# Performance work log

Measured on AMD Instinct MI355X. Metric: run time of the kernel, lower is better.

The kernel has to match this reference:

```python
import jax, jax.numpy as jnp
import numpy as np

BLOCK = 32  # GGUF Q8_0 block size
O, I = 4096, 4096
NB = I // BLOCK  # blocks per output row
B, S = 2, 2048


def setup_inputs() -> dict:
    key = jax.random.key(0)
    k1, k2, k3, k4 = jax.random.split(key, 4)
    x = jax.random.normal(k1, (B, S, I), dtype=jnp.float32)
    # signed int8 quants stored as int32 (values in [-128, 127])
    q_weight = jax.random.randint(k2, (O, I), 0, 256, dtype=jnp.int32) - 128
    # per-block fp scales (small positive, as produced by Q8_0 quantization)
    scales = jax.random.uniform(k3, (O, NB), dtype=jnp.float32) * 0.02 + 1e-4
    bias = jax.random.normal(k4, (O,), dtype=jnp.float32)
    return {"x": x, "q_weight": q_weight, "scales": scales, "bias": bias}


def dequantize(q_weight, scales, dtype):
    # q_weight: [O, I] int, scales: [O, NB] float; block-wise dequant (Q8_0)
    q = q_weight.reshape(O, NB, BLOCK).astype(dtype)
    w = q * scales.astype(dtype)[:, :, None]
    return w.reshape(O, I)  # [O, I]


def reference(x, q_weight, scales, bias):
    # cast_bias_weight: dequantize weight/bias to the input dtype, then linear
    dtype = x.dtype
    w = dequantize(q_weight, scales, dtype)          # [O, I]
    y = jnp.einsum('bsi,oi->bso', x, w) + bias.astype(dtype)
    return y
```

## Files before the change

kernel.cpp:

```cpp
#include <hip/hip_runtime.h>
#include <hip/hip_bf16.h>
#include <stdint.h>


#define M_DIM 4096
#define N_DIM 4096
#define K_DIM 4096
#define NB_SC 128

#define BM 256
#define BN 256
#define BKB 128
#define NT (K_DIM / BKB)
#define TILE_B (BM * BKB)

typedef __attribute__((ext_vector_type(4))) int i32x4;

__device__ __forceinline__ void gload_lds16(const void* gsrc, void* ldsdst) {
  __builtin_amdgcn_global_load_lds(
      (__attribute__((address_space(1))) void*)(uintptr_t)gsrc,
      (__attribute__((address_space(3))) void*)(uint32_t)(uintptr_t)ldsdst,
      16, 0, 0);
}

__device__ __forceinline__ int pack4(int a, int b, int c, int d) {
  return (a & 255) | ((b & 255) << 8) | ((c & 255) << 16) | ((d & 255) << 24);
}


__global__ void prep_kernel(const float* __restrict__ x, const int* __restrict__ q,
                            const float* __restrict__ sc,
                            char* __restrict__ xb, char* __restrict__ wb,
                            float* __restrict__ sxv, float* __restrict__ swv) {
  __shared__ float red[4];
  const int b = blockIdx.x;
  const int t = threadIdx.x;
  if (b < 4096) {
    const float4* row = (const float4*)(x + (size_t)b * K_DIM);
    float4 v[4];
    float m = 0.f;
#pragma unroll
    for (int i = 0; i < 4; ++i) {
      v[i] = row[t * 4 + i];
      m = fmaxf(m, fmaxf(fmaxf(fabsf(v[i].x), fabsf(v[i].y)),
                         fmaxf(fabsf(v[i].z), fabsf(v[i].w))));
    }
#pragma unroll
    for (int off = 32; off >= 1; off >>= 1) m = fmaxf(m, __shfl_xor(m, off, 64));
    if ((t & 63) == 0) red[t >> 6] = m;
    __syncthreads();
    m = fmaxf(fmaxf(red[0], red[1]), fmaxf(red[2], red[3]));
    const float inv = (m > 0.f) ? 127.0f / m : 0.f;
    int4 o;
    o.x = pack4(__float2int_rn(v[0].x * inv), __float2int_rn(v[0].y * inv),
                __float2int_rn(v[0].z * inv), __float2int_rn(v[0].w * inv));
    o.y = pack4(__float2int_rn(v[1].x * inv), __float2int_rn(v[1].y * inv),
                __float2int_rn(v[1].z * inv), __float2int_rn(v[1].w * inv));
    o.z = pack4(__float2int_rn(v[2].x * inv), __float2int_rn(v[2].y * inv),
                __float2int_rn(v[2].z * inv), __float2int_rn(v[2].w * inv));
    o.w = pack4(__float2int_rn(v[3].x * inv), __float2int_rn(v[3].y * inv),
                __float2int_rn(v[3].z * inv), __float2int_rn(v[3].w * inv));
    ((int4*)(xb + (size_t)b * K_DIM))[t] = o;
    if (t == 0) sxv[b] = m / 127.0f;
  } else {
    const int o_row = b - 4096;
    float m = sc[o_row * NB_SC + (t & 127)];
#pragma unroll
    for (int off = 32; off >= 1; off >>= 1) m = fmaxf(m, __shfl_xor(m, off, 64));
    if ((t & 63) == 0) red[t >> 6] = m;
    __syncthreads();
    m = fmaxf(fmaxf(red[0], red[1]), fmaxf(red[2], red[3]));
    const float ratio = sc[o_row * NB_SC + (t >> 1)] / m;
    const int4* qp = (const int4*)(q + (size_t)o_row * K_DIM);
    int4 qv[4];
#pragma unroll
    for (int i = 0; i < 4; ++i) qv[i] = qp[t * 4 + i];
    int4 ov;
    ov.x = pack4(__float2int_rn((float)qv[0].x * ratio), __float2int_rn((float)qv[0].y * ratio),
                 __float2int_rn((float)qv[0].z * ratio), __float2int_rn((float)qv[0].w * ratio));
    ov.y = pack4(__float2int_rn((float)qv[1].x * ratio), __float2int_rn((float)qv[1].y * ratio),
                 __float2int_rn((float)qv[1].z * ratio), __float2int_rn((float)qv[1].w * ratio));
    ov.z = pack4(__float2int_rn((float)qv[2].x * ratio), __float2int_rn((float)qv[2].y * ratio),
                 __float2int_rn((float)qv[2].z * ratio), __float2int_rn((float)qv[2].w * ratio));
    ov.w = pack4(__float2int_rn((float)qv[3].x * ratio), __float2int_rn((float)qv[3].y * ratio),
                 __float2int_rn((float)qv[3].z * ratio), __float2int_rn((float)qv[3].w * ratio));
    ((int4*)(wb + (size_t)o_row * K_DIM))[t] = ov;
    if (t == 0) swv[o_row] = m;
  }
}


__device__ __forceinline__ void stage_half(const char* __restrict__ pX,
                                           char* lds, int hr0, int ktb, int w) {
#pragma unroll
  for (int j = 0; j < 2; ++j) {
    gload_lds16(pX + (size_t)(hr0 + j * 8) * K_DIM + ktb,
                lds + (hr0 + w * 16 + j * 8) * BKB);
  }
}

template <int BUF, int Q>
__device__ __forceinline__ void read_aq(const char* pa0, const char* pa1,
                                        i32x4 (&af)[2][2]) {
#pragma unroll
  for (int j = 0; j < 2; ++j) {
    af[j][0] = *(const i32x4*)(pa0 + BUF * TILE_B + (Q * 32 + j * 16) * BKB);
    af[j][1] = *(const i32x4*)(pa1 + BUF * TILE_B + (Q * 32 + j * 16) * BKB);
  }
}

template <int BUF, int NI>
__device__ __forceinline__ void read_bpair(const char* pb0, const char* pb1,
                                           i32x4 (&bf)[4][2]) {
#pragma unroll
  for (int ni = NI; ni < NI + 2; ++ni) {
    bf[ni][0] = *(const i32x4*)(pb0 + BUF * TILE_B + ni * 16 * BKB);
    bf[ni][1] = *(const i32x4*)(pb1 + BUF * TILE_B + ni * 16 * BKB);
  }
}

__device__ __forceinline__ void mfma_quad(const i32x4 (&af)[2][2], const i32x4 (&bf)[4][2],
                                          i32x4 (&acc)[8][4], int q0) {
  __builtin_amdgcn_s_setprio(1);
#pragma unroll
  for (int q = 0; q < 2; ++q)
#pragma unroll
    for (int ni = 0; ni < 4; ++ni)
#pragma unroll
      for (int kk = 0; kk < 2; ++kk)
        acc[q0 + q][ni] =
            __builtin_amdgcn_mfma_i32_16x16x64_i8(af[q][kk], bf[ni][kk], acc[q0 + q][ni], 0, 0, 0);
  __builtin_amdgcn_s_setprio(0);
}

template <int BUF, int MODE>
__device__ __forceinline__ void ktile(const char* pa0, const char* pa1,
                                      const char* pb0, const char* pb1,
                                      const char* __restrict__ pA,
                                      const char* __restrict__ pB,
                                      char* AsB, char* BsB,
                                      int ktb, int w,
                                      i32x4 (&acc)[8][4],
                                      i32x4 (&bf_cur)[4][2], i32x4 (&bf_nxt)[4][2],
                                      i32x4 (&a0_cur)[2][2], i32x4 (&a0_nxt)[2][2]) {
  char* Anw = AsB + (BUF ^ 1) * TILE_B;
  char* Bw  = BsB + BUF * TILE_B;

  i32x4 a1[2][2], a2[2][2], a3[2][2];

  read_aq<BUF, 1>(pa0, pa1, a1);
  if (MODE < 2) {
    stage_half(pA, Anw, 0, ktb + BKB, w);
    stage_half(pA, Anw, 128, ktb + BKB, w);
  }
  __builtin_amdgcn_sched_barrier(0);
  mfma_quad(a0_cur, bf_cur, acc, 0);
  __builtin_amdgcn_s_barrier();

  read_aq<BUF, 2>(pa0, pa1, a2);
  if (MODE == 0) stage_half(pB, Bw, 0, ktb + 2 * BKB, w);
  __builtin_amdgcn_sched_barrier(0);
  mfma_quad(a1, bf_cur, acc, 2);
  if (MODE == 0)
    asm volatile("s_waitcnt vmcnt(6)" ::: "memory");
  else if (MODE == 1)
    asm volatile("s_waitcnt vmcnt(4)" ::: "memory");
  __builtin_amdgcn_s_barrier();

  read_aq<BUF, 3>(pa0, pa1, a3);
  if (MODE < 2) read_bpair<(BUF ^ 1) & 1, 0>(pb0, pb1, bf_nxt);
  if (MODE == 0) stage_half(pB, Bw, 128, ktb + 2 * BKB, w);
  __builtin_amdgcn_sched_barrier(0);
  mfma_quad(a2, bf_cur, acc, 4);
  __builtin_amdgcn_s_barrier();

  if (MODE == 0)
    asm volatile("s_waitcnt vmcnt(4)" ::: "memory");
  else if (MODE == 1)
    asm volatile("s_waitcnt vmcnt(0)" ::: "memory");
  if (MODE < 2) {
    read_bpair<(BUF ^ 1) & 1, 2>(pb0, pb1, bf_nxt);
    read_aq<(BUF ^ 1) & 1, 0>(pa0, pa1, a0_nxt);
  }
  __builtin_amdgcn_sched_barrier(0);
  mfma_quad(a3, bf_cur, acc, 6);
  __builtin_amdgcn_s_barrier();
}

__global__ __launch_bounds__(512, 2) void gemm256(const char* __restrict__ A,
                                                  const char* __restrict__ B,
                                                  const float* __restrict__ sxv,
                                                  const float* __restrict__ swv,
                                                  const float* __restrict__ bias,
                                                  float* __restrict__ C) {
  __shared__ char AsB[2 * TILE_B];
  __shared__ char BsB[2 * TILE_B];

  const int tid = threadIdx.x;
  const int w = tid >> 6;
  const int l = tid & 63;
  const int wm = w >> 2;
  const int wn = w & 3;
  const int frow = l & 15;
  const int fkb = (l >> 4) * 16;

  const int bid = blockIdx.x;
  const int cpx = gridDim.x >> 3;
  const int swz = (bid & 7) * cpx + (bid >> 3);
  const int bm0 = (swz >> 4) * BM;
  const int bn0 = (swz & 15) * BN;

  const int fr7 = frow & 7;
  const int sw0 = (((fkb) >> 4) ^ fr7) << 4;
  const int sw1 = (((fkb + 64) >> 4) ^ fr7) << 4;
  const char* pa0 = (const char*)AsB + (wm * 128 + frow) * BKB + sw0;
  const char* pa1 = (const char*)AsB + (wm * 128 + frow) * BKB + sw1;
  const char* pb0 = (const char*)BsB + (wn * 64 + frow) * BKB + sw0;
  const char* pb1 = (const char*)BsB + (wn * 64 + frow) * BKB + sw1;

  const int sr = l >> 3;
  const int skp = ((l & 7) ^ sr) << 4;
  const char* pA = A + (size_t)(bm0 + w * 16 + sr) * K_DIM + skp;
  const char* pB = B + (size_t)(bn0 + w * 16 + sr) * K_DIM + skp;

  i32x4 acc[8][4] = {};
  i32x4 bf0[4][2], bf1[4][2];
  i32x4 a00[2][2], a01[2][2];

  stage_half(pB, BsB, 0, 0, w);
  stage_half(pB, BsB, 128, 0, w);
  stage_half(pA, AsB, 0, 0, w);
  stage_half(pA, AsB, 128, 0, w);
  stage_half(pB, BsB + TILE_B, 0, BKB, w);
  stage_half(pB, BsB + TILE_B, 128, BKB, w);
  asm volatile("s_waitcnt vmcnt(4)" ::: "memory");
  __builtin_amdgcn_s_barrier();
  read_bpair<0, 0>(pb0, pb1, bf0);
  read_bpair<0, 2>(pb0, pb1, bf0);
  read_aq<0, 0>(pa0, pa1, a00);

  for (int t = 0; t < NT - 2; t += 2) {
    ktile<0, 0>(pa0, pa1, pb0, pb1, pA, pB, AsB, BsB, t * BKB, w,
                acc, bf0, bf1, a00, a01);
    ktile<1, 0>(pa0, pa1, pb0, pb1, pA, pB, AsB, BsB, (t + 1) * BKB, w,
                acc, bf1, bf0, a01, a00);
  }
  ktile<0, 1>(pa0, pa1, pb0, pb1, pA, pB, AsB, BsB, (NT - 2) * BKB, w,
              acc, bf0, bf1, a00, a01);
  ktile<1, 2>(pa0, pa1, pb0, pb1, pA, pB, AsB, BsB, (NT - 1) * BKB, w,
              acc, bf1, bf0, a01, a00);

#pragma unroll
  for (int ni = 0; ni < 4; ++ni) {
    const int n = bn0 + wn * 64 + ni * 16 + (l & 15);
    const float swn = swv[n];
    const float bv = bias[n];
#pragma unroll
    for (int mi = 0; mi < 8; ++mi) {
      const int mbase = bm0 + wm * 128 + mi * 16 + (l >> 4) * 4;
#pragma unroll
      for (int r = 0; r < 4; ++r)
        C[(size_t)(mbase + r) * N_DIM + n] =
            (float)acc[mi][ni][r] * (swn * sxv[mbase + r]) + bv;
    }
  }
}


__global__ void naive_kernel(const float* __restrict__ x, const int* __restrict__ q,
                             const float* __restrict__ sc, const float* __restrict__ bias,
                             float* __restrict__ out) {
  size_t idx = (size_t)blockIdx.x * blockDim.x + threadIdx.x;
  if (idx >= (size_t)M_DIM * N_DIM) return;
  int n = (int)(idx & (N_DIM - 1));
  size_t m = idx >> 12;
  float acc = 0.f;
  for (int k = 0; k < K_DIM; k += 32) {
    float s = sc[n * NB_SC + (k >> 5)];
    float part = 0.f;
    for (int j = 0; j < 32; ++j)
      part += x[m * K_DIM + k + j] * (float)q[(size_t)n * K_DIM + k + j];
    acc += part * s;
  }
  out[idx] = acc + bias[n];
}


extern "C" void kernel_launch(void* const* d_in, const int* in_sizes, int n_in,
                              void* d_out, int out_size, void* d_ws, size_t ws_size,
                              hipStream_t stream) {
  const float* x    = (const float*)d_in[0];
  const int*   q    = (const int*)d_in[1];
  const float* sc   = (const float*)d_in[2];
  const float* bias = (const float*)d_in[3];
  float* out = (float*)d_out;

  const size_t elems = (size_t)M_DIM * K_DIM;
  const size_t need  = 2 * elems + 2 * 4096 * sizeof(float);

  if (ws_size >= need) {
    char* xb = (char*)d_ws;
    char* wb = xb + elems;
    float* sxv = (float*)(wb + elems);
    float* swv = sxv + 4096;
    hipLaunchKernelGGL(prep_kernel, dim3(8192), dim3(256), 0, stream,
                       x, q, sc, xb, wb, sxv, swv);
    hipLaunchKernelGGL(gemm256, dim3((M_DIM / BM) * (N_DIM / BN)), dim3(512), 0, stream,
                       xb, wb, sxv, swv, bias, out);
  } else {
    hipLaunchKernelGGL(naive_kernel, dim3((M_DIM * N_DIM) / 256), dim3(256), 0, stream,
                       x, q, sc, bias, out);
  }
}
```

Before: 92.28 us.

## Restructure int8 GEMM k-tile pipeline to drop cross-tile register prefetch

Rewrites the per-k-tile schedule so that B fragments and the first A quarter are read from LDS at the start of each tile, rather than being prefetched into double-buffered registers during the previous tile. The A-tile global-to-LDS staging is split into halves placed at different phases, with an extra half staged in the prologue, and every phase now ends with a barrier plus a full lgkmcnt wait. The aim is to cut VGPR pressure and simplify the software pipeline. The cost is exposed LDS-read latency at the start of each tile and more waits, which could serialize LDS reads with MFMA work.

```diff
diff --git a/kernel.cpp b/kernel.cpp
--- a/kernel.cpp
+++ b/kernel.cpp
@@ -109,11 +109,11 @@
   }
 }
 
-template <int BUF, int NI>
-__device__ __forceinline__ void read_bpair(const char* pb0, const char* pb1,
-                                           i32x4 (&bf)[4][2]) {
-#pragma unroll
-  for (int ni = NI; ni < NI + 2; ++ni) {
+template <int BUF>
+__device__ __forceinline__ void read_ball(const char* pb0, const char* pb1,
+                                          i32x4 (&bf)[4][2]) {
+#pragma unroll
+  for (int ni = 0; ni < 4; ++ni) {
     bf[ni][0] = *(const i32x4*)(pb0 + BUF * TILE_B + ni * 16 * BKB);
     bf[ni][1] = *(const i32x4*)(pb1 + BUF * TILE_B + ni * 16 * BKB);
   }
@@ -132,6 +132,11 @@
             __builtin_amdgcn_mfma_i32_16x16x64_i8(af[q][kk], bf[ni][kk], acc[q0 + q][ni], 0, 0, 0);
   __builtin_amdgcn_s_setprio(0);
 }
+
+#define PHASE_SYNC()                                   \
+  __builtin_amdgcn_s_barrier();                        \
+  asm volatile("s_waitcnt lgkmcnt(0)" ::: "memory");   \
+  __builtin_amdgcn_sched_barrier(0)
 
 template <int BUF, int MODE>
 __device__ __forceinline__ void ktile(const char* pa0, const char* pa1,
@@ -140,51 +145,51 @@
                                       const char* __restrict__ pB,
                                       char* AsB, char* BsB,
                                       int ktb, int w,
-                                      i32x4 (&acc)[8][4],
-                                      i32x4 (&bf_cur)[4][2], i32x4 (&bf_nxt)[4][2],
-                                      i32x4 (&a0_cur)[2][2], i32x4 (&a0_nxt)[2][2]) {
+                                      i32x4 (&acc)[8][4]) {
   char* Anw = AsB + (BUF ^ 1) * TILE_B;
+  char* Aw  = AsB + BUF * TILE_B;
   char* Bw  = BsB + BUF * TILE_B;
 
-  i32x4 a1[2][2], a2[2][2], a3[2][2];
-
-  read_aq<BUF, 1>(pa0, pa1, a1);
-  if (MODE < 2) {
-    stage_half(pA, Anw, 0, ktb + BKB, w);
-    stage_half(pA, Anw, 128, ktb + BKB, w);
-  }
-  __builtin_amdgcn_sched_barrier(0);
-  mfma_quad(a0_cur, bf_cur, acc, 0);
-  __builtin_amdgcn_s_barrier();
-
-  read_aq<BUF, 2>(pa0, pa1, a2);
-  if (MODE == 0) stage_half(pB, Bw, 0, ktb + 2 * BKB, w);
-  __builtin_amdgcn_sched_barrier(0);
-  mfma_quad(a1, bf_cur, acc, 2);
-  if (MODE == 0)
-    asm volatile("s_waitcnt vmcnt(6)" ::: "memory");
-  else if (MODE == 1)
-    asm volatile("s_waitcnt vmcnt(4)" ::: "memory");
-  __builtin_amdgcn_s_barrier();
-
-  read_aq<BUF, 3>(pa0, pa1, a3);
-  if (MODE < 2) read_bpair<(BUF ^ 1) & 1, 0>(pb0, pb1, bf_nxt);
-  if (MODE == 0) stage_half(pB, Bw, 128, ktb + 2 * BKB, w);
-  __builtin_amdgcn_sched_barrier(0);
-  mfma_quad(a2, bf_cur, acc, 4);
-  __builtin_amdgcn_s_barrier();
-
-  if (MODE == 0)
-    asm volatile("s_waitcnt vmcnt(4)" ::: "memory");
-  else if (MODE == 1)
-    asm volatile("s_waitcnt vmcnt(0)" ::: "memory");
-  if (MODE < 2) {
-    read_bpair<(BUF ^ 1) & 1, 2>(pb0, pb1, bf_nxt);
-    read_aq<(BUF ^ 1) & 1, 0>(pa0, pa1, a0_nxt);
-  }
-  __builtin_amdgcn_sched_barrier(0);
-  mfma_quad(a3, bf_cur, acc, 6);
-  __builtin_amdgcn_s_barrier();
+  i32x4 bf[4][2];
+
+  {
+    i32x4 a0[2][2];
+    read_ball<BUF>(pb0, pb1, bf);
+    read_aq<BUF, 0>(pa0, pa1, a0);
+    if (MODE < 2) stage_half(pA, Anw, 128, ktb + BKB, w);
+    asm volatile("s_waitcnt lgkmcnt(8)" ::: "memory");
+    PHASE_SYNC();
+    mfma_quad(a0, bf, acc, 0);
+    __builtin_amdgcn_s_barrier();
+  }
+  {
+    i32x4 a1[2][2];
+    read_aq<BUF, 1>(pa0, pa1, a1);
+    if (MODE == 0) stage_half(pB, Bw, 0, ktb + 2 * BKB, w);
+    PHASE_SYNC();
+    mfma_quad(a1, bf, acc, 2);
+    __builtin_amdgcn_s_barrier();
+  }
+  {
+    i32x4 a2[2][2];
+    read_aq<BUF, 2>(pa0, pa1, a2);
+    if (MODE == 0) stage_half(pB, Bw, 128, ktb + 2 * BKB, w);
+    PHASE_SYNC();
+    mfma_quad(a2, bf, acc, 4);
+    __builtin_amdgcn_s_barrier();
+  }
+  {
+    i32x4 a3[2][2];
+    read_aq<BUF, 3>(pa0, pa1, a3);
+    if (MODE == 0) stage_half(pA, Aw, 0, ktb + 2 * BKB, w);
+    PHASE_SYNC();
+    mfma_quad(a3, bf, acc, 6);
+    if (MODE == 0)
+      asm volatile("s_waitcnt vmcnt(6)" ::: "memory");
+    else if (MODE == 1)
+      asm volatile("s_waitcnt vmcnt(0)" ::: "memory");
+    __builtin_amdgcn_s_barrier();
+  }
 }
 
 __global__ __launch_bounds__(512, 2) void gemm256(const char* __restrict__ A,
@@ -224,8 +229,6 @@
   const char* pB = B + (size_t)(bn0 + w * 16 + sr) * K_DIM + skp;
 
   i32x4 acc[8][4] = {};
-  i32x4 bf0[4][2], bf1[4][2];
-  i32x4 a00[2][2], a01[2][2];
 
   stage_half(pB, BsB, 0, 0, w);
   stage_half(pB, BsB, 128, 0, w);
@@ -233,22 +236,16 @@
   stage_half(pA, AsB, 128, 0, w);
   stage_half(pB, BsB + TILE_B, 0, BKB, w);
   stage_half(pB, BsB + TILE_B, 128, BKB, w);
-  asm volatile("s_waitcnt vmcnt(4)" ::: "memory");
+  stage_half(pA, AsB + TILE_B, 0, BKB, w);
+  asm volatile("s_waitcnt vmcnt(6)" ::: "memory");
   __builtin_amdgcn_s_barrier();
-  read_bpair<0, 0>(pb0, pb1, bf0);
-  read_bpair<0, 2>(pb0, pb1, bf0);
-  read_aq<0, 0>(pa0, pa1, a00);
 
   for (int t = 0; t < NT - 2; t += 2) {
-    ktile<0, 0>(pa0, pa1, pb0, pb1, pA, pB, AsB, BsB, t * BKB, w,
-                acc, bf0, bf1, a00, a01);
-    ktile<1, 0>(pa0, pa1, pb0, pb1, pA, pB, AsB, BsB, (t + 1) * BKB, w,
-                acc, bf1, bf0, a01, a00);
-  }
-  ktile<0, 1>(pa0, pa1, pb0, pb1, pA, pB, AsB, BsB, (NT - 2) * BKB, w,
-              acc, bf0, bf1, a00, a01);
-  ktile<1, 2>(pa0, pa1, pb0, pb1, pA, pB, AsB, BsB, (NT - 1) * BKB, w,
-              acc, bf1, bf0, a01, a00);
+    ktile<0, 0>(pa0, pa1, pb0, pb1, pA, pB, AsB, BsB, t * BKB, w, acc);
+    ktile<1, 0>(pa0, pa1, pb0, pb1, pA, pB, AsB, BsB, (t + 1) * BKB, w, acc);
+  }
+  ktile<0, 1>(pa0, pa1, pb0, pb1, pA, pB, AsB, BsB, (NT - 2) * BKB, w, acc);
+  ktile<1, 2>(pa0, pa1, pb0, pb1, pA, pB, AsB, BsB, (NT - 1) * BKB, w, acc);
 
 #pragma unroll
   for (int ni = 0; ni < 4; ++ni) {
```

New measurement: 94.64 us. 1.03x slower.
